# Kernel optimization log

Hardware: AMD Instinct MI355X
Metric: run time of the kernel (lower is better)

Reference implementation:

```python
import jax, jax.numpy as jnp
import numpy as np

N = 100000        # nodes
M = 100000        # hyperedges
IN_F = 128
OUT_F = 128
MAX_ARITY = 8
ALPHA = 0.2       # LeakyReLU negative slope
NEG_INF = -9e15   # padding value used by the original module


def _xavier_uniform(key, shape, gain=1.414):
    fan_in, fan_out = shape[0], shape[-1]
    bound = gain * np.sqrt(6.0 / (fan_in + fan_out))
    return jax.random.uniform(key, shape, jnp.float32, -bound, bound)


def setup_inputs() -> dict:
    key = jax.random.key(0)
    k = jax.random.split(key, 6)
    node_embs = jax.random.normal(k[0], (N, IN_F), jnp.float32)
    edge_embs = jax.random.normal(k[1], (M, IN_F), jnp.float32)  # only M=shape[0] is used
    edge_list = jax.random.randint(k[2], (M, MAX_ARITY), 0, N, jnp.int32)
    arity = jax.random.randint(k[3], (M,), 1, MAX_ARITY + 1, jnp.int32)
    edge_mask = jnp.arange(MAX_ARITY)[None, :] < arity[:, None]  # [M, A] bool
    W1 = _xavier_uniform(k[4], (IN_F, OUT_F))
    a1 = _xavier_uniform(k[5], (OUT_F, 1))
    return {"node_embs": node_embs, "edge_embs": edge_embs, "edge_list": edge_list,
            "edge_mask": edge_mask, "W1": W1, "a1": a1}


def reference(node_embs, edge_embs, edge_list, edge_mask, W1, a1):
    # Wh: [N, OUT_F]
    Wh = node_embs @ W1
    # Gather per-hyperedge node features: [M, A, OUT_F]
    g = Wh[edge_list]
    # Per-edge scores: leakyrelu(Wh[s]) @ a1, padded with -9e15 -> [M, A, 1]
    s = jnp.einsum('maf,fo->mao', jax.nn.leaky_relu(g, negative_slope=ALPHA), a1)
    s = jnp.where(edge_mask[..., None], s, NEG_INF)
    attention = jax.nn.softmax(s, axis=1)                 # softmax over arity slots
    Whs = jnp.where(edge_mask[..., None], g, 0.0)         # zero-padded features
    # Faithful to original: torch.sum(..., dim=0) sums over edges -> [A, OUT_F]
    return jnp.sum(attention * Whs, axis=0)
```

## Files before the change

### kernel.cpp

```cpp
#include <hip/hip_runtime.h>

typedef unsigned int uint32;
typedef __attribute__((ext_vector_type(8))) short short8v;
typedef __attribute__((ext_vector_type(4))) float f32x4;

__device__ __forceinline__ unsigned short f2bf(float f) {
  unsigned u = __float_as_uint(f);
  return (unsigned short)((u + 0x7FFFu + ((u >> 16) & 1u)) >> 16);
}
__device__ __forceinline__ float bfl(unsigned x) { return __uint_as_float(x << 16); }
__device__ __forceinline__ float bfh(unsigned x) { return __uint_as_float(x & 0xFFFF0000u); }

__global__ __launch_bounds__(256) void k0_zero_detect(const uint32* __restrict__ md,
                                                      int* __restrict__ flag,
                                                      float4* __restrict__ W8v, int n4) {
  const int t = blockIdx.x * blockDim.x + threadIdx.x;
  for (int i = t; i < n4; i += gridDim.x * blockDim.x)
    W8v[i] = (float4){0.f, 0.f, 0.f, 0.f};
  if (blockIdx.x == 0 && threadIdx.x < 64) {
    bool ok4 = true;
    for (int i = threadIdx.x; i < 1024; i += 64) {
      uint32 v = md[i];
      if (!(v == 0u || v == 1u || v == 0x3F800000u)) ok4 = false;
    }
    bool all4 = __all(ok4);
    if (threadIdx.x == 0) *flag = all4 ? 4 : 1;
  }
}

__global__ __launch_bounds__(256) void k1_mfma(const float* __restrict__ X,
                                               const float* __restrict__ W,
                                               const float* __restrict__ a1,
                                               unsigned short* __restrict__ Wh,
                                               float* __restrict__ sigma,
                                               int N) {
  __shared__ short sB[2048 * 8];
  const int tid = threadIdx.x;
  for (int i = tid; i < 2048; i += 256) {
    const int frag = i >> 6, ln = i & 63;
    const int kt = frag >> 3, ct = frag & 7, p = ln >> 4, q = ln & 15;
    short8v v;
    #pragma unroll
    for (int j = 0; j < 8; ++j)
      v[j] = (short)f2bf(W[(kt * 32 + p * 8 + j) * 128 + ct * 16 + q]);
    *(short8v*)&sB[i * 8] = v;
  }
  __syncthreads();

  const int lane = tid & 63;
  const int p = lane >> 4, q = lane & 15;
  float a1v[8];
  #pragma unroll
  for (int ct = 0; ct < 8; ++ct) a1v[ct] = a1[ct * 16 + q];

  const int wave = blockIdx.x * 4 + (tid >> 6);
  const int nwaves = gridDim.x * 4;
  const int nstrips = (N + 15) >> 4;

  for (int s = wave; s < nstrips; s += nwaves) {
    const int row = s * 16 + q;
    const int rclamp = row < N ? row : (N - 1);
    const float* xr = X + (size_t)rclamp * 128 + p * 8;
    float4 L[8];
    #pragma unroll
    for (int kt = 0; kt < 4; ++kt) {
      L[2 * kt]     = *(const float4*)(xr + kt * 32);
      L[2 * kt + 1] = *(const float4*)(xr + kt * 32 + 4);
    }
    short8v A[4];
    #pragma unroll
    for (int kt = 0; kt < 4; ++kt) {
      #pragma unroll
      for (int j = 0; j < 4; ++j) {
        A[kt][j]     = (short)f2bf((&L[2 * kt].x)[j]);
        A[kt][j + 4] = (short)f2bf((&L[2 * kt + 1].x)[j]);
      }
    }
    f32x4 acc[8];
    #pragma unroll
    for (int ct = 0; ct < 8; ++ct) acc[ct] = (f32x4){0.f, 0.f, 0.f, 0.f};
    #pragma unroll
    for (int kt = 0; kt < 4; ++kt) {
      #pragma unroll
      for (int ct = 0; ct < 8; ++ct) {
        short8v b = *(const short8v*)&sB[((kt * 8 + ct) * 64 + lane) * 8];
        acc[ct] = __builtin_amdgcn_mfma_f32_16x16x32_bf16(A[kt], b, acc[ct], 0, 0, 0);
      }
    }
    const int r0 = s * 16 + p * 4;
    #pragma unroll
    for (int ct = 0; ct < 8; ++ct) {
      #pragma unroll
      for (int r = 0; r < 4; ++r) {
        const int rr = r0 + r;
        if (rr < N) Wh[(size_t)rr * 128 + ct * 16 + q] = f2bf(acc[ct][r]);
      }
    }
    #pragma unroll
    for (int r = 0; r < 4; ++r) {
      float tsum = 0.f;
      #pragma unroll
      for (int ct = 0; ct < 8; ++ct) {
        const float v = acc[ct][r];
        tsum += fmaxf(v, 0.2f * v) * a1v[ct];
      }
      tsum += __shfl_xor(tsum, 1);
      tsum += __shfl_xor(tsum, 2);
      tsum += __shfl_xor(tsum, 4);
      tsum += __shfl_xor(tsum, 8);
      const int rr = r0 + r;
      if (q == r && rr < N) sigma[rr] = tsum;
    }
  }
}

template <int MSZ>
__device__ __forceinline__ void k2a_body(const int* __restrict__ elist,
                                         const void* __restrict__ maskp,
                                         const float* __restrict__ sigma,
                                         float* __restrict__ W8, int m) {
  const int4 ia = ((const int4*)elist)[m * 2];
  const int4 ib = ((const int4*)elist)[m * 2 + 1];
  const int idx[8] = {ia.x, ia.y, ia.z, ia.w, ib.x, ib.y, ib.z, ib.w};
  int vld[8];
  if (MSZ == 4) {
    const int4 ma = ((const int4*)maskp)[m * 2];
    const int4 mb = ((const int4*)maskp)[m * 2 + 1];
    vld[0] = ma.x; vld[1] = ma.y; vld[2] = ma.z; vld[3] = ma.w;
    vld[4] = mb.x; vld[5] = mb.y; vld[6] = mb.z; vld[7] = mb.w;
  } else {
    const uint2 u = ((const uint2*)maskp)[m];
    vld[0] = u.x & 0xFF; vld[1] = (u.x >> 8) & 0xFF;
    vld[2] = (u.x >> 16) & 0xFF; vld[3] = u.x >> 24;
    vld[4] = u.y & 0xFF; vld[5] = (u.y >> 8) & 0xFF;
    vld[6] = (u.y >> 16) & 0xFF; vld[7] = u.y >> 24;
  }
  float sg[8];
  #pragma unroll
  for (int a = 0; a < 8; ++a) sg[a] = sigma[idx[a]];
  float mx = -3.0e38f;
  #pragma unroll
  for (int a = 0; a < 8; ++a) mx = fmaxf(mx, vld[a] ? sg[a] : -3.0e38f);
  float ev[8];
  float dn = 0.f;
  #pragma unroll
  for (int a = 0; a < 8; ++a) {
    ev[a] = vld[a] ? __expf(sg[a] - mx) : 0.f;
    dn += ev[a];
  }
  const float inv = __fdividef(1.f, dn);
  #pragma unroll
  for (int a = 0; a < 8; ++a)
    if (vld[a]) atomicAdd(&W8[(size_t)idx[a] * 8 + a], ev[a] * inv);
}

__global__ __launch_bounds__(256) void k2a_edges(const int* __restrict__ elist,
                                                 const void* __restrict__ maskp,
                                                 const float* __restrict__ sigma,
                                                 const int* __restrict__ flag,
                                                 float* __restrict__ W8, int M) {
  const int m = blockIdx.x * 256 + threadIdx.x;
  if (m >= M) return;
  if (*flag == 4) k2a_body<4>(elist, maskp, sigma, W8, m);
  else            k2a_body<1>(elist, maskp, sigma, W8, m);
}

__global__ __launch_bounds__(256) void k2b_nodes(const uint32* __restrict__ Wh32,
                                                 const float* __restrict__ W8,
                                                 float* __restrict__ partial, int N) {
  __shared__ float sAcc[4][1024];
  const int lane = threadIdx.x & 63, wv = threadIdx.x >> 6;
  const int wave = blockIdx.x * 4 + wv, nw = gridDim.x * 4;
  float acc[16];
  #pragma unroll
  for (int j = 0; j < 16; ++j) acc[j] = 0.f;

  for (int n = wave; n < N; n += 2 * nw) {
    const int n2 = n + nw;
    const uint32 d0 = Wh32[(size_t)n * 64 + lane];
    const float4 wa0 = *(const float4*)&W8[(size_t)n * 8];
    const float4 wb0 = *(const float4*)&W8[(size_t)n * 8 + 4];
    uint32 d1 = 0;
    float4 wa1 = {0.f, 0.f, 0.f, 0.f}, wb1 = {0.f, 0.f, 0.f, 0.f};
    if (n2 < N) {
      d1 = Wh32[(size_t)n2 * 64 + lane];
      wa1 = *(const float4*)&W8[(size_t)n2 * 8];
      wb1 = *(const float4*)&W8[(size_t)n2 * 8 + 4];
    }
    const float lo0 = bfl(d0), hi0 = bfh(d0);
    acc[0]  = fmaf(wa0.x, lo0, acc[0]);  acc[1]  = fmaf(wa0.x, hi0, acc[1]);
    acc[2]  = fmaf(wa0.y, lo0, acc[2]);  acc[3]  = fmaf(wa0.y, hi0, acc[3]);
    acc[4]  = fmaf(wa0.z, lo0, acc[4]);  acc[5]  = fmaf(wa0.z, hi0, acc[5]);
    acc[6]  = fmaf(wa0.w, lo0, acc[6]);  acc[7]  = fmaf(wa0.w, hi0, acc[7]);
    acc[8]  = fmaf(wb0.x, lo0, acc[8]);  acc[9]  = fmaf(wb0.x, hi0, acc[9]);
    acc[10] = fmaf(wb0.y, lo0, acc[10]); acc[11] = fmaf(wb0.y, hi0, acc[11]);
    acc[12] = fmaf(wb0.z, lo0, acc[12]); acc[13] = fmaf(wb0.z, hi0, acc[13]);
    acc[14] = fmaf(wb0.w, lo0, acc[14]); acc[15] = fmaf(wb0.w, hi0, acc[15]);
    const float lo1 = bfl(d1), hi1 = bfh(d1);
    acc[0]  = fmaf(wa1.x, lo1, acc[0]);  acc[1]  = fmaf(wa1.x, hi1, acc[1]);
    acc[2]  = fmaf(wa1.y, lo1, acc[2]);  acc[3]  = fmaf(wa1.y, hi1, acc[3]);
    acc[4]  = fmaf(wa1.z, lo1, acc[4]);  acc[5]  = fmaf(wa1.z, hi1, acc[5]);
    acc[6]  = fmaf(wa1.w, lo1, acc[6]);  acc[7]  = fmaf(wa1.w, hi1, acc[7]);
    acc[8]  = fmaf(wb1.x, lo1, acc[8]);  acc[9]  = fmaf(wb1.x, hi1, acc[9]);
    acc[10] = fmaf(wb1.y, lo1, acc[10]); acc[11] = fmaf(wb1.y, hi1, acc[11]);
    acc[12] = fmaf(wb1.z, lo1, acc[12]); acc[13] = fmaf(wb1.z, hi1, acc[13]);
    acc[14] = fmaf(wb1.w, lo1, acc[14]); acc[15] = fmaf(wb1.w, hi1, acc[15]);
  }

  #pragma unroll
  for (int a = 0; a < 8; ++a) {
    sAcc[wv][a * 128 + 2 * lane]     = acc[2 * a];
    sAcc[wv][a * 128 + 2 * lane + 1] = acc[2 * a + 1];
  }
  __syncthreads();
  const int c = threadIdx.x * 4;
  float4 s = {0.f, 0.f, 0.f, 0.f};
  #pragma unroll
  for (int w = 0; w < 4; ++w) {
    const float4 v = *(const float4*)&sAcc[w][c];
    s.x += v.x; s.y += v.y; s.z += v.z; s.w += v.w;
  }
  *(float4*)&partial[(size_t)blockIdx.x * 1024 + c] = s;
}

__global__ __launch_bounds__(64) void k3_reduce(const float* __restrict__ partial,
                                                float* __restrict__ out, int nb) {
  const int c = blockIdx.x * 64 + threadIdx.x;
  float s = 0.f;
  #pragma unroll 16
  for (int j = 0; j < nb; ++j) s += partial[(size_t)j * 1024 + c];
  out[c] = s;
}

extern "C" void kernel_launch(void* const* d_in, const int* in_sizes, int n_in,
                              void* d_out, int out_size, void* d_ws, size_t ws_size,
                              hipStream_t stream) {
  const float* node  = (const float*)d_in[0];
  const int* elist   = (const int*)d_in[2];
  const void* maskp  = (const void*)d_in[3];
  const float* W1    = (const float*)d_in[4];
  const float* a1    = (const float*)d_in[5];
  float* out         = (float*)d_out;

  const int N = in_sizes[0] / 128;
  const int M = in_sizes[2] / 8;
  const int K2B_BLOCKS = 256;

  char* ws = (char*)d_ws;
  unsigned short* Wh = (unsigned short*)ws;
  size_t off = (size_t)N * 256;
  float* sigma = (float*)(ws + off);  off += (size_t)N * 4;
  off = (off + 255) & ~(size_t)255;
  float* W8 = (float*)(ws + off);     off += (size_t)N * 32;
  off = (off + 255) & ~(size_t)255;
  float* partial = (float*)(ws + off); off += (size_t)K2B_BLOCKS * 1024 * 4;
  int* flag = (int*)(ws + off);

  k0_zero_detect<<<256, 256, 0, stream>>>((const uint32*)maskp, flag,
                                          (float4*)W8, N * 2);
  k1_mfma<<<784, 256, 0, stream>>>(node, W1, a1, Wh, sigma, N);
  k2a_edges<<<(M + 255) / 256, 256, 0, stream>>>(elist, maskp, sigma, flag, W8, M);
  k2b_nodes<<<K2B_BLOCKS, 256, 0, stream>>>((const uint32*)Wh, W8, partial, N);
  k3_reduce<<<16, 64, 0, stream>>>(partial, out, K2B_BLOCKS);
}
```

Measured before the change: 117.3 us.

## Fuse all stages into one persistent kernel with software grid barriers

Replaces the five separate launches (zero/detect, GEMM+score, edge softmax scatter, node reduction, final reduce) with a single persistent kernel sized to two blocks per CU. Stages are separated by an atomic-counter grid barrier, and the final cross-block reduction uses atomicAdd into the output instead of a partial buffer plus reduce kernel. Zeroing moves to hipMemsetAsync. The aim is to remove launch gaps and tail effects, at the cost of less parallelism per phase, spin-barrier overhead, and a reliance on all blocks being co-resident. The barrier has a spin timeout that could silently break correctness.

Result: slower. 318.9 us (+171.9%).

```diff
diff --git a/kernel.cpp b/kernel.cpp
--- a/kernel.cpp
+++ b/kernel.cpp
@@ -11,114 +11,32 @@
 __device__ __forceinline__ float bfl(unsigned x) { return __uint_as_float(x << 16); }
 __device__ __forceinline__ float bfh(unsigned x) { return __uint_as_float(x & 0xFFFF0000u); }
 
-__global__ __launch_bounds__(256) void k0_zero_detect(const uint32* __restrict__ md,
-                                                      int* __restrict__ flag,
-                                                      float4* __restrict__ W8v, int n4) {
-  const int t = blockIdx.x * blockDim.x + threadIdx.x;
-  for (int i = t; i < n4; i += gridDim.x * blockDim.x)
-    W8v[i] = (float4){0.f, 0.f, 0.f, 0.f};
-  if (blockIdx.x == 0 && threadIdx.x < 64) {
-    bool ok4 = true;
-    for (int i = threadIdx.x; i < 1024; i += 64) {
-      uint32 v = md[i];
-      if (!(v == 0u || v == 1u || v == 0x3F800000u)) ok4 = false;
-    }
-    bool all4 = __all(ok4);
-    if (threadIdx.x == 0) *flag = all4 ? 4 : 1;
-  }
-}
-
-__global__ __launch_bounds__(256) void k1_mfma(const float* __restrict__ X,
-                                               const float* __restrict__ W,
-                                               const float* __restrict__ a1,
-                                               unsigned short* __restrict__ Wh,
-                                               float* __restrict__ sigma,
-                                               int N) {
-  __shared__ short sB[2048 * 8];
-  const int tid = threadIdx.x;
-  for (int i = tid; i < 2048; i += 256) {
-    const int frag = i >> 6, ln = i & 63;
-    const int kt = frag >> 3, ct = frag & 7, p = ln >> 4, q = ln & 15;
-    short8v v;
-    #pragma unroll
-    for (int j = 0; j < 8; ++j)
-      v[j] = (short)f2bf(W[(kt * 32 + p * 8 + j) * 128 + ct * 16 + q]);
-    *(short8v*)&sB[i * 8] = v;
-  }
+__device__ __forceinline__ void grid_barrier(int* cnt, int* gen) {
   __syncthreads();
-
-  const int lane = tid & 63;
-  const int p = lane >> 4, q = lane & 15;
-  float a1v[8];
-  #pragma unroll
-  for (int ct = 0; ct < 8; ++ct) a1v[ct] = a1[ct * 16 + q];
-
-  const int wave = blockIdx.x * 4 + (tid >> 6);
-  const int nwaves = gridDim.x * 4;
-  const int nstrips = (N + 15) >> 4;
-
-  for (int s = wave; s < nstrips; s += nwaves) {
-    const int row = s * 16 + q;
-    const int rclamp = row < N ? row : (N - 1);
-    const float* xr = X + (size_t)rclamp * 128 + p * 8;
-    float4 L[8];
-    #pragma unroll
-    for (int kt = 0; kt < 4; ++kt) {
-      L[2 * kt]     = *(const float4*)(xr + kt * 32);
-      L[2 * kt + 1] = *(const float4*)(xr + kt * 32 + 4);
-    }
-    short8v A[4];
-    #pragma unroll
-    for (int kt = 0; kt < 4; ++kt) {
-      #pragma unroll
-      for (int j = 0; j < 4; ++j) {
-        A[kt][j]     = (short)f2bf((&L[2 * kt].x)[j]);
-        A[kt][j + 4] = (short)f2bf((&L[2 * kt + 1].x)[j]);
-      }
-    }
-    f32x4 acc[8];
-    #pragma unroll
-    for (int ct = 0; ct < 8; ++ct) acc[ct] = (f32x4){0.f, 0.f, 0.f, 0.f};
-    #pragma unroll
-    for (int kt = 0; kt < 4; ++kt) {
-      #pragma unroll
-      for (int ct = 0; ct < 8; ++ct) {
-        short8v b = *(const short8v*)&sB[((kt * 8 + ct) * 64 + lane) * 8];
-        acc[ct] = __builtin_amdgcn_mfma_f32_16x16x32_bf16(A[kt], b, acc[ct], 0, 0, 0);
-      }
-    }
-    const int r0 = s * 16 + p * 4;
-    #pragma unroll
-    for (int ct = 0; ct < 8; ++ct) {
-      #pragma unroll
-      for (int r = 0; r < 4; ++r) {
-        const int rr = r0 + r;
-        if (rr < N) Wh[(size_t)rr * 128 + ct * 16 + q] = f2bf(acc[ct][r]);
-      }
-    }
-    #pragma unroll
-    for (int r = 0; r < 4; ++r) {
-      float tsum = 0.f;
-      #pragma unroll
-      for (int ct = 0; ct < 8; ++ct) {
-        const float v = acc[ct][r];
-        tsum += fmaxf(v, 0.2f * v) * a1v[ct];
-      }
-      tsum += __shfl_xor(tsum, 1);
-      tsum += __shfl_xor(tsum, 2);
-      tsum += __shfl_xor(tsum, 4);
-      tsum += __shfl_xor(tsum, 8);
-      const int rr = r0 + r;
-      if (q == r && rr < N) sigma[rr] = tsum;
-    }
-  }
+  if (threadIdx.x == 0) {
+    __threadfence();
+    int g = __hip_atomic_load(gen, __ATOMIC_RELAXED, __HIP_MEMORY_SCOPE_AGENT);
+    int arrived = __hip_atomic_fetch_add(cnt, 1, __ATOMIC_ACQ_REL, __HIP_MEMORY_SCOPE_AGENT);
+    if (arrived == (int)gridDim.x - 1) {
+      __hip_atomic_store(cnt, 0, __ATOMIC_RELAXED, __HIP_MEMORY_SCOPE_AGENT);
+      __hip_atomic_fetch_add(gen, 1, __ATOMIC_ACQ_REL, __HIP_MEMORY_SCOPE_AGENT);
+    } else {
+      int spins = 0;
+      while (__hip_atomic_load(gen, __ATOMIC_ACQUIRE, __HIP_MEMORY_SCOPE_AGENT) == g) {
+        __builtin_amdgcn_s_sleep(8);
+        if (++spins > (1 << 22)) break;
+      }
+    }
+    __threadfence();
+  }
+  __syncthreads();
 }
 
 template <int MSZ>
-__device__ __forceinline__ void k2a_body(const int* __restrict__ elist,
-                                         const void* __restrict__ maskp,
-                                         const float* __restrict__ sigma,
-                                         float* __restrict__ W8, int m) {
+__device__ __forceinline__ void edge_attend(const int* __restrict__ elist,
+                                            const void* __restrict__ maskp,
+                                            const float* __restrict__ sigma,
+                                            float* __restrict__ W8, int m) {
   const int4 ia = ((const int4*)elist)[m * 2];
   const int4 ib = ((const int4*)elist)[m * 2 + 1];
   const int idx[8] = {ia.x, ia.y, ia.z, ia.w, ib.x, ib.y, ib.z, ib.w};
@@ -154,82 +72,182 @@
     if (vld[a]) atomicAdd(&W8[(size_t)idx[a] * 8 + a], ev[a] * inv);
 }
 
-__global__ __launch_bounds__(256) void k2a_edges(const int* __restrict__ elist,
-                                                 const void* __restrict__ maskp,
-                                                 const float* __restrict__ sigma,
-                                                 const int* __restrict__ flag,
-                                                 float* __restrict__ W8, int M) {
-  const int m = blockIdx.x * 256 + threadIdx.x;
-  if (m >= M) return;
-  if (*flag == 4) k2a_body<4>(elist, maskp, sigma, W8, m);
-  else            k2a_body<1>(elist, maskp, sigma, W8, m);
-}
-
-__global__ __launch_bounds__(256) void k2b_nodes(const uint32* __restrict__ Wh32,
-                                                 const float* __restrict__ W8,
-                                                 float* __restrict__ partial, int N) {
-  __shared__ float sAcc[4][1024];
-  const int lane = threadIdx.x & 63, wv = threadIdx.x >> 6;
-  const int wave = blockIdx.x * 4 + wv, nw = gridDim.x * 4;
-  float acc[16];
-  #pragma unroll
-  for (int j = 0; j < 16; ++j) acc[j] = 0.f;
-
-  for (int n = wave; n < N; n += 2 * nw) {
-    const int n2 = n + nw;
-    const uint32 d0 = Wh32[(size_t)n * 64 + lane];
-    const float4 wa0 = *(const float4*)&W8[(size_t)n * 8];
-    const float4 wb0 = *(const float4*)&W8[(size_t)n * 8 + 4];
-    uint32 d1 = 0;
-    float4 wa1 = {0.f, 0.f, 0.f, 0.f}, wb1 = {0.f, 0.f, 0.f, 0.f};
-    if (n2 < N) {
-      d1 = Wh32[(size_t)n2 * 64 + lane];
-      wa1 = *(const float4*)&W8[(size_t)n2 * 8];
-      wb1 = *(const float4*)&W8[(size_t)n2 * 8 + 4];
-    }
-    const float lo0 = bfl(d0), hi0 = bfh(d0);
-    acc[0]  = fmaf(wa0.x, lo0, acc[0]);  acc[1]  = fmaf(wa0.x, hi0, acc[1]);
-    acc[2]  = fmaf(wa0.y, lo0, acc[2]);  acc[3]  = fmaf(wa0.y, hi0, acc[3]);
-    acc[4]  = fmaf(wa0.z, lo0, acc[4]);  acc[5]  = fmaf(wa0.z, hi0, acc[5]);
-    acc[6]  = fmaf(wa0.w, lo0, acc[6]);  acc[7]  = fmaf(wa0.w, hi0, acc[7]);
-    acc[8]  = fmaf(wb0.x, lo0, acc[8]);  acc[9]  = fmaf(wb0.x, hi0, acc[9]);
-    acc[10] = fmaf(wb0.y, lo0, acc[10]); acc[11] = fmaf(wb0.y, hi0, acc[11]);
-    acc[12] = fmaf(wb0.z, lo0, acc[12]); acc[13] = fmaf(wb0.z, hi0, acc[13]);
-    acc[14] = fmaf(wb0.w, lo0, acc[14]); acc[15] = fmaf(wb0.w, hi0, acc[15]);
-    const float lo1 = bfl(d1), hi1 = bfh(d1);
-    acc[0]  = fmaf(wa1.x, lo1, acc[0]);  acc[1]  = fmaf(wa1.x, hi1, acc[1]);
-    acc[2]  = fmaf(wa1.y, lo1, acc[2]);  acc[3]  = fmaf(wa1.y, hi1, acc[3]);
-    acc[4]  = fmaf(wa1.z, lo1, acc[4]);  acc[5]  = fmaf(wa1.z, hi1, acc[5]);
-    acc[6]  = fmaf(wa1.w, lo1, acc[6]);  acc[7]  = fmaf(wa1.w, hi1, acc[7]);
-    acc[8]  = fmaf(wb1.x, lo1, acc[8]);  acc[9]  = fmaf(wb1.x, hi1, acc[9]);
-    acc[10] = fmaf(wb1.y, lo1, acc[10]); acc[11] = fmaf(wb1.y, hi1, acc[11]);
-    acc[12] = fmaf(wb1.z, lo1, acc[12]); acc[13] = fmaf(wb1.z, hi1, acc[13]);
-    acc[14] = fmaf(wb1.w, lo1, acc[14]); acc[15] = fmaf(wb1.w, hi1, acc[15]);
-  }
-
-  #pragma unroll
-  for (int a = 0; a < 8; ++a) {
-    sAcc[wv][a * 128 + 2 * lane]     = acc[2 * a];
-    sAcc[wv][a * 128 + 2 * lane + 1] = acc[2 * a + 1];
+__global__ __launch_bounds__(256, 2) void fused_all(
+    const float* __restrict__ X, const float* __restrict__ W,
+    const float* __restrict__ a1, const int* __restrict__ elist,
+    const void* __restrict__ maskp, unsigned short* __restrict__ Wh,
+    float* __restrict__ sigma, float* __restrict__ W8,
+    int* __restrict__ bar, int* __restrict__ flag,
+    float* __restrict__ out, int N, int M) {
+  __shared__ short sB[2048 * 8];
+  const int tid = threadIdx.x;
+  const int gtid = blockIdx.x * 256 + tid;
+  const int nthreads = gridDim.x * 256;
+  const int lane = tid & 63;
+  const int wv = tid >> 6;
+
+  if (blockIdx.x == 0 && tid < 64) {
+    const uint32* md = (const uint32*)maskp;
+    bool ok4 = true;
+    for (int i = tid; i < 1024; i += 64) {
+      uint32 v = md[i];
+      if (!(v == 0u || v == 1u || v == 0x3F800000u)) ok4 = false;
+    }
+    bool all4 = __all(ok4);
+    if (tid == 0)
+      __hip_atomic_store(flag, all4 ? 4 : 1, __ATOMIC_RELAXED, __HIP_MEMORY_SCOPE_AGENT);
+  }
+
+  for (int i = tid; i < 2048; i += 256) {
+    const int frag = i >> 6, ln = i & 63;
+    const int kt = frag >> 3, ct = frag & 7, p = ln >> 4, q = ln & 15;
+    short8v v;
+    #pragma unroll
+    for (int j = 0; j < 8; ++j)
+      v[j] = (short)f2bf(W[(kt * 32 + p * 8 + j) * 128 + ct * 16 + q]);
+    *(short8v*)&sB[i * 8] = v;
   }
   __syncthreads();
-  const int c = threadIdx.x * 4;
-  float4 s = {0.f, 0.f, 0.f, 0.f};
-  #pragma unroll
-  for (int w = 0; w < 4; ++w) {
-    const float4 v = *(const float4*)&sAcc[w][c];
-    s.x += v.x; s.y += v.y; s.z += v.z; s.w += v.w;
-  }
-  *(float4*)&partial[(size_t)blockIdx.x * 1024 + c] = s;
-}
-
-__global__ __launch_bounds__(64) void k3_reduce(const float* __restrict__ partial,
-                                                float* __restrict__ out, int nb) {
-  const int c = blockIdx.x * 64 + threadIdx.x;
-  float s = 0.f;
-  #pragma unroll 16
-  for (int j = 0; j < nb; ++j) s += partial[(size_t)j * 1024 + c];
-  out[c] = s;
+  {
+    const int p = lane >> 4, q = lane & 15;
+    float a1v[8];
+    #pragma unroll
+    for (int ct = 0; ct < 8; ++ct) a1v[ct] = a1[ct * 16 + q];
+    const int wave = blockIdx.x * 4 + wv;
+    const int nwaves = gridDim.x * 4;
+    const int nstrips = (N + 15) >> 4;
+    for (int s = wave; s < nstrips; s += nwaves) {
+      const int row = s * 16 + q;
+      const int rclamp = row < N ? row : (N - 1);
+      const float* xr = X + (size_t)rclamp * 128 + p * 8;
+      float4 L[8];
+      #pragma unroll
+      for (int kt = 0; kt < 4; ++kt) {
+        L[2 * kt]     = *(const float4*)(xr + kt * 32);
+        L[2 * kt + 1] = *(const float4*)(xr + kt * 32 + 4);
+      }
+      short8v A[4];
+      #pragma unroll
+      for (int kt = 0; kt < 4; ++kt) {
+        #pragma unroll
+        for (int j = 0; j < 4; ++j) {
+          A[kt][j]     = (short)f2bf((&L[2 * kt].x)[j]);
+          A[kt][j + 4] = (short)f2bf((&L[2 * kt + 1].x)[j]);
+        }
+      }
+      f32x4 acc[8];
+      #pragma unroll
+      for (int ct = 0; ct < 8; ++ct) acc[ct] = (f32x4){0.f, 0.f, 0.f, 0.f};
+      #pragma unroll
+      for (int kt = 0; kt < 4; ++kt) {
+        #pragma unroll
+        for (int ct = 0; ct < 8; ++ct) {
+          short8v b = *(const short8v*)&sB[((kt * 8 + ct) * 64 + lane) * 8];
+          acc[ct] = __builtin_amdgcn_mfma_f32_16x16x32_bf16(A[kt], b, acc[ct], 0, 0, 0);
+        }
+      }
+      const int r0 = s * 16 + p * 4;
+      #pragma unroll
+      for (int ct = 0; ct < 8; ++ct) {
+        #pragma unroll
+        for (int r = 0; r < 4; ++r) {
+          const int rr = r0 + r;
+          if (rr < N) Wh[(size_t)rr * 128 + ct * 16 + q] = f2bf(acc[ct][r]);
+        }
+      }
+      #pragma unroll
+      for (int r = 0; r < 4; ++r) {
+        float tsum = 0.f;
+        #pragma unroll
+        for (int ct = 0; ct < 8; ++ct) {
+          const float v = acc[ct][r];
+          tsum += fmaxf(v, 0.2f * v) * a1v[ct];
+        }
+        tsum += __shfl_xor(tsum, 1);
+        tsum += __shfl_xor(tsum, 2);
+        tsum += __shfl_xor(tsum, 4);
+        tsum += __shfl_xor(tsum, 8);
+        const int rr = r0 + r;
+        if (q == r && rr < N) sigma[rr] = tsum;
+      }
+    }
+  }
+
+  grid_barrier(bar, bar + 16);
+
+  {
+    const int msz = __hip_atomic_load(flag, __ATOMIC_RELAXED, __HIP_MEMORY_SCOPE_AGENT);
+    if (msz == 4) {
+      for (int m = gtid; m < M; m += nthreads)
+        edge_attend<4>(elist, maskp, sigma, W8, m);
+    } else {
+      for (int m = gtid; m < M; m += nthreads)
+        edge_attend<1>(elist, maskp, sigma, W8, m);
+    }
+  }
+
+  grid_barrier(bar, bar + 16);
+
+  {
+    const uint32* Wh32 = (const uint32*)Wh;
+    float* sAcc = (float*)sB;
+    const int wave = blockIdx.x * 4 + wv;
+    const int nw = gridDim.x * 4;
+    float acc[16];
+    #pragma unroll
+    for (int j = 0; j < 16; ++j) acc[j] = 0.f;
+
+    for (int n = wave; n < N; n += 2 * nw) {
+      const int n2 = n + nw;
+      const uint32 d0 = Wh32[(size_t)n * 64 + lane];
+      const float4 wa0 = *(const float4*)&W8[(size_t)n * 8];
+      const float4 wb0 = *(const float4*)&W8[(size_t)n * 8 + 4];
+      uint32 d1 = 0;
+      float4 wa1 = {0.f, 0.f, 0.f, 0.f}, wb1 = {0.f, 0.f, 0.f, 0.f};
+      if (n2 < N) {
+        d1 = Wh32[(size_t)n2 * 64 + lane];
+        wa1 = *(const float4*)&W8[(size_t)n2 * 8];
+        wb1 = *(const float4*)&W8[(size_t)n2 * 8 + 4];
+      }
+      const float lo0 = bfl(d0), hi0 = bfh(d0);
+      acc[0]  = fmaf(wa0.x, lo0, acc[0]);  acc[1]  = fmaf(wa0.x, hi0, acc[1]);
+      acc[2]  = fmaf(wa0.y, lo0, acc[2]);  acc[3]  = fmaf(wa0.y, hi0, acc[3]);
+      acc[4]  = fmaf(wa0.z, lo0, acc[4]);  acc[5]  = fmaf(wa0.z, hi0, acc[5]);
+      acc[6]  = fmaf(wa0.w, lo0, acc[6]);  acc[7]  = fmaf(wa0.w, hi0, acc[7]);
+      acc[8]  = fmaf(wb0.x, lo0, acc[8]);  acc[9]  = fmaf(wb0.x, hi0, acc[9]);
+      acc[10] = fmaf(wb0.y, lo0, acc[10]); acc[11] = fmaf(wb0.y, hi0, acc[11]);
+      acc[12] = fmaf(wb0.z, lo0, acc[12]); acc[13] = fmaf(wb0.z, hi0, acc[13]);
+      acc[14] = fmaf(wb0.w, lo0, acc[14]); acc[15] = fmaf(wb0.w, hi0, acc[15]);
+      const float lo1 = bfl(d1), hi1 = bfh(d1);
+      acc[0]  = fmaf(wa1.x, lo1, acc[0]);  acc[1]  = fmaf(wa1.x, hi1, acc[1]);
+      acc[2]  = fmaf(wa1.y, lo1, acc[2]);  acc[3]  = fmaf(wa1.y, hi1, acc[3]);
+      acc[4]  = fmaf(wa1.z, lo1, acc[4]);  acc[5]  = fmaf(wa1.z, hi1, acc[5]);
+      acc[6]  = fmaf(wa1.w, lo1, acc[6]);  acc[7]  = fmaf(wa1.w, hi1, acc[7]);
+      acc[8]  = fmaf(wb1.x, lo1, acc[8]);  acc[9]  = fmaf(wb1.x, hi1, acc[9]);
+      acc[10] = fmaf(wb1.y, lo1, acc[10]); acc[11] = fmaf(wb1.y, hi1, acc[11]);
+      acc[12] = fmaf(wb1.z, lo1, acc[12]); acc[13] = fmaf(wb1.z, hi1, acc[13]);
+      acc[14] = fmaf(wb1.w, lo1, acc[14]); acc[15] = fmaf(wb1.w, hi1, acc[15]);
+    }
+
+    __syncthreads();
+    #pragma unroll
+    for (int a = 0; a < 8; ++a) {
+      sAcc[wv * 1024 + a * 128 + 2 * lane]     = acc[2 * a];
+      sAcc[wv * 1024 + a * 128 + 2 * lane + 1] = acc[2 * a + 1];
+    }
+    __syncthreads();
+    const int c = tid * 4;
+    float4 s = {0.f, 0.f, 0.f, 0.f};
+    #pragma unroll
+    for (int w = 0; w < 4; ++w) {
+      const float4 v = *(const float4*)&sAcc[w * 1024 + c];
+      s.x += v.x; s.y += v.y; s.z += v.z; s.w += v.w;
+    }
+    atomicAdd(&out[c], s.x);
+    atomicAdd(&out[c + 1], s.y);
+    atomicAdd(&out[c + 2], s.z);
+    atomicAdd(&out[c + 3], s.w);
+  }
 }
 
 extern "C" void kernel_launch(void* const* d_in, const int* in_sizes, int n_in,
@@ -242,24 +260,30 @@
   const float* a1    = (const float*)d_in[5];
   float* out         = (float*)d_out;
 
-  const int N = in_sizes[0] / 128;
-  const int M = in_sizes[2] / 8;
-  const int K2B_BLOCKS = 256;
+  int N = in_sizes[0] / 128;
+  int M = in_sizes[2] / 8;
 
   char* ws = (char*)d_ws;
   unsigned short* Wh = (unsigned short*)ws;
   size_t off = (size_t)N * 256;
   float* sigma = (float*)(ws + off);  off += (size_t)N * 4;
   off = (off + 255) & ~(size_t)255;
-  float* W8 = (float*)(ws + off);     off += (size_t)N * 32;
-  off = (off + 255) & ~(size_t)255;
-  float* partial = (float*)(ws + off); off += (size_t)K2B_BLOCKS * 1024 * 4;
-  int* flag = (int*)(ws + off);
-
-  k0_zero_detect<<<256, 256, 0, stream>>>((const uint32*)maskp, flag,
-                                          (float4*)W8, N * 2);
-  k1_mfma<<<784, 256, 0, stream>>>(node, W1, a1, Wh, sigma, N);
-  k2a_edges<<<(M + 255) / 256, 256, 0, stream>>>(elist, maskp, sigma, flag, W8, M);
-  k2b_nodes<<<K2B_BLOCKS, 256, 0, stream>>>((const uint32*)Wh, W8, partial, N);
-  k3_reduce<<<16, 64, 0, stream>>>(partial, out, K2B_BLOCKS);
-}
+  float* W8 = (float*)(ws + off);
+  const size_t zeroBytes = (size_t)N * 32 + 256;
+  int* bar  = (int*)(ws + off + (size_t)N * 32);
+  int* flag = bar + 32;
+  off += zeroBytes;
+
+  int dev = 0;
+  (void)hipGetDevice(&dev);
+  int cu = 0;
+  (void)hipDeviceGetAttribute(&cu, hipDeviceAttributeMultiprocessorCount, dev);
+  if (cu <= 0) cu = 256;
+  int grid = 2 * cu;
+  if (grid > 512) grid = 512;
+
+  (void)hipMemsetAsync(W8, 0, zeroBytes, stream);
+  (void)hipMemsetAsync(out, 0, (size_t)out_size * 4, stream);
+  fused_all<<<grid, 256, 0, stream>>>(node, W1, a1, elist, maskp, Wh, sigma, W8,
+                                      bar, flag, out, N, M);
+}
```
